# Performance work log

Hardware: AMD Instinct MI355X
Metric: run time of the kernel (lower is better)

The kernel has to match this reference:

```python
import jax, jax.numpy as jnp
import numpy as np

# 8 directional difference stencils (N, S, E, W, NE, SE, SW, NW), OIHW [8,1,3,3]
_WINDOWS = np.array([
    [[0, 1, 0], [0, -1, 0], [0, 0, 0]],
    [[0, 0, 0], [0, -1, 0], [0, 1, 0]],
    [[0, 0, 0], [0, -1, 1], [0, 0, 0]],
    [[0, 0, 0], [1, -1, 0], [0, 0, 0]],
    [[0, 0, 1], [0, -1, 0], [0, 0, 0]],
    [[0, 0, 0], [0, -1, 0], [0, 0, 1]],
    [[0, 0, 0], [0, -1, 0], [1, 0, 0]],
    [[1, 0, 0], [0, -1, 0], [0, 0, 0]],
], dtype=np.float32).reshape(8, 1, 3, 3)

ITERATIONS = 30  # int(self.iterations.item()) with init value 30.0


def setup_inputs() -> dict:
    key = jax.random.key(0)
    k1, k2, k3 = jax.random.split(key, 3)
    x = jax.random.normal(k1, (32, 3, 512, 512), dtype=jnp.float32)
    W_expand = jax.random.normal(k2, (3, 3, 1, 1), dtype=jnp.float32) * 0.3
    b_expand = jax.random.normal(k3, (3,), dtype=jnp.float32) * 0.1
    return {
        "x": x,
        "delta": jnp.float32(0.1),
        "kappa": jnp.float32(15.0),
        "W_expand": W_expand,
        "b_expand": b_expand,
    }


def reference(x, delta, kappa, W_expand, b_expand):
    K = jnp.asarray(_WINDOWS)  # [8,1,3,3]
    # axial directions weight 1, diagonal directions weight 1/(sqrt(2))^2 = 0.5
    dir_w = jnp.array([1.0, 1.0, 1.0, 1.0, 0.5, 0.5, 0.5, 0.5],
                      dtype=x.dtype).reshape(1, 8, 1, 1)

    # RGB -> luminance, [B,1,H,W]
    u = (0.299 * x[:, 0] + 0.587 * x[:, 1] + 0.114 * x[:, 2])[:, None]

    def step(u, _):
        # all 8 directional gradients in one grouped conv: [B,8,H,W]
        nabla = jax.lax.conv_general_dilated(
            u, K, window_strides=(1, 1), padding='SAME',
            dimension_numbers=('NCHW', 'OIHW', 'NCHW'))
        diff = 1.0 / (1.0 + (nabla / kappa) ** 2)  # Perona-Malik diffusivity
        upd = jnp.sum(dir_w * diff * nabla, axis=1, keepdims=True)
        return u + delta * upd, None

    u, _ = jax.lax.scan(step, u, None, length=ITERATIONS)

    # repeat to 3 channels then 1x1 conv (expand_channels)
    u_rgb = jnp.repeat(u, 3, axis=1)  # [B,3,H,W]
    out = jnp.einsum('oi,bihw->bohw', W_expand[:, :, 0, 0], u_rgb)
    out = out + b_expand[None, :, None, None]
    return out
```

## Files before the change

### kernel.cpp

```cpp
#include <hip/hip_runtime.h>

#define BATCH 32
#define HGT 512
#define WID 512
#define PLANE (HGT * WID)
#define NPIX (BATCH * PLANE)
#define BSTRIDE (3 * PLANE)
#define NQUAD (NPIX / 4)

#define RSLAB 32
#define SLABS (HGT / RSLAB)
#define FBLOCKS (BATCH * SLABS)
#define FT 512
#define NW 8

__device__ __forceinline__ float4 ld4(const float* p) {
    return *reinterpret_cast<const float4*>(p);
}
__device__ __forceinline__ void st4(float* p, float4 v) {
    *reinterpret_cast<float4*>(p) = v;
}

__device__ __forceinline__ float pm_flux(float d, float ik2) {
    return d * __builtin_amdgcn_rcpf(fmaf(d * d, ik2, 1.f));
}

struct RowState {
    float m[10];
    float pV[8], pSE[9], pSW[9];
};

__device__ __forceinline__ void load_row10(const float* __restrict__ buf, int row, int o,
                                           float m[10]) {
    const float* p = buf + row * WID + (o << 3);
    float4 lo = ld4(p);
    float4 hi = ld4(p + 4);
    float le = __shfl_up(hi.w, 1);
    float re = __shfl_down(lo.x, 1);
    m[0] = (o == 0) ? 0.f : le;
    m[1] = lo.x; m[2] = lo.y; m[3] = lo.z; m[4] = lo.w;
    m[5] = hi.x; m[6] = hi.y; m[7] = hi.z; m[8] = hi.w;
    m[9] = (o == 63) ? 0.f : re;
}

__device__ __forceinline__ void level10(const float a[10], const float b[10],
                                        float vF[8], float seF[9], float swF[9],
                                        float ik2) {
#pragma unroll
    for (int j = 0; j < 8; ++j) vF[j] = pm_flux(b[j + 1] - a[j + 1], ik2);
#pragma unroll
    for (int i = 0; i < 9; ++i) seF[i] = pm_flux(b[i + 1] - a[i], ik2);
#pragma unroll
    for (int i = 0; i < 9; ++i) swF[i] = pm_flux(b[i] - a[i + 1], ik2);
}

template <int MODE, int S>
__global__ __launch_bounds__(FT) __attribute__((amdgpu_waves_per_eu(4, 4)))
void pm_fusedk(const float* __restrict__ src, int sstr,
               float* __restrict__ dst, int dstr,
               const float* __restrict__ pdelta, const float* __restrict__ pkappa,
               const float* __restrict__ Wexp, const float* __restrict__ bexp) {
    constexpr int LR = RSLAB + 2 * S;
    __shared__ float buf[LR * WID];

    const int img  = blockIdx.x >> 4;
    const int slab = blockIdx.x & (SLABS - 1);
    const int H0   = slab * RSLAB;
    const int tid  = threadIdx.x;
    const int wave = tid >> 6;
    const int o    = tid & 63;

    const float delta = *pdelta;
    const float kappa = *pkappa;
    const float ik2 = __builtin_amdgcn_rcpf(kappa * kappa);

    const float* sb = src + (size_t)img * sstr;
    for (int i = tid; i < LR * (WID / 4); i += FT) {
        int row = i >> 7;
        int q   = i & 127;
        int g = H0 - S + row;
        float4 v = make_float4(0.f, 0.f, 0.f, 0.f);
        if ((unsigned)g < (unsigned)HGT) {
            const float* p = sb + g * WID + (q << 2);
            if (MODE == 0) {
                float4 r = ld4(p), gg = ld4(p + PLANE), bb = ld4(p + 2 * PLANE);
                v.x = fmaf(0.299f, r.x, fmaf(0.587f, gg.x, 0.114f * bb.x));
                v.y = fmaf(0.299f, r.y, fmaf(0.587f, gg.y, 0.114f * bb.y));
                v.z = fmaf(0.299f, r.z, fmaf(0.587f, gg.z, 0.114f * bb.z));
                v.w = fmaf(0.299f, r.w, fmaf(0.587f, gg.w, 0.114f * bb.w));
            } else {
                v = ld4(p);
            }
        }
        st4(buf + row * WID + (q << 2), v);
    }
    __syncthreads();

    float s0c = 0.f, s1c = 0.f, s2c = 0.f, b0c = 0.f, b1c = 0.f, b2c = 0.f;
    if (MODE == 2) {
        s0c = Wexp[0] + Wexp[1] + Wexp[2];
        s1c = Wexp[3] + Wexp[4] + Wexp[5];
        s2c = Wexp[6] + Wexp[7] + Wexp[8];
        b0c = bexp[0]; b1c = bexp[1]; b2c = bexp[2];
    }

    float* db = dst + (size_t)img * dstr;

    for (int s = 0; s < S; ++s) {
        const int tot = LR - 2 - 2 * s;
        const int bse = tot >> 3, rem = tot & 7;
        const int n   = bse + (wave < rem ? 1 : 0);
        const int st0 = s + 1 + wave * bse + (wave < rem ? wave : rem);
        const bool fin = (s == S - 1);

        RowState A, B;
        {
            float a10[10];
            load_row10(buf, st0 - 1, o, a10);
            load_row10(buf, st0, o, A.m);
            level10(a10, A.m, A.pV, A.pSE, A.pSW, ik2);
        }
        float4 f0 = make_float4(0, 0, 0, 0), f1 = f0, l0 = f0, l1 = f0;

        auto do_row = [&](RowState& CUR, RowState& NEXT, int i) {
            load_row10(buf, st0 + i + 1, o, NEXT.m);
            float hF[9];
#pragma unroll
            for (int t = 0; t < 9; ++t) hF[t] = pm_flux(CUR.m[t + 1] - CUR.m[t], ik2);
            level10(CUR.m, NEXT.m, NEXT.pV, NEXT.pSE, NEXT.pSW, ik2);
            float o8[8];
#pragma unroll
            for (int j = 0; j < 8; ++j) {
                float axial = NEXT.pV[j] - CUR.pV[j] + hF[j + 1] - hF[j];
                float diag  = NEXT.pSE[j + 1] + NEXT.pSW[j]
                            - CUR.pSE[j] - CUR.pSW[j + 1];
                o8[j] = fmaf(delta, fmaf(0.5f, diag, axial), CUR.m[j + 1]);
            }
            const int g = H0 - S + st0 + i;
            if ((unsigned)g >= (unsigned)HGT) {
#pragma unroll
                for (int j = 0; j < 8; ++j) o8[j] = 0.f;
            }
            float4 r0 = make_float4(o8[0], o8[1], o8[2], o8[3]);
            float4 r1 = make_float4(o8[4], o8[5], o8[6], o8[7]);
            if (fin) {
                float* p = db + (size_t)g * WID + (o << 3);
                if (MODE == 2) {
                    st4(p, make_float4(fmaf(s0c, r0.x, b0c), fmaf(s0c, r0.y, b0c),
                                       fmaf(s0c, r0.z, b0c), fmaf(s0c, r0.w, b0c)));
                    st4(p + 4, make_float4(fmaf(s0c, r1.x, b0c), fmaf(s0c, r1.y, b0c),
                                           fmaf(s0c, r1.z, b0c), fmaf(s0c, r1.w, b0c)));
                    st4(p + PLANE,
                        make_float4(fmaf(s1c, r0.x, b1c), fmaf(s1c, r0.y, b1c),
                                    fmaf(s1c, r0.z, b1c), fmaf(s1c, r0.w, b1c)));
                    st4(p + PLANE + 4,
                        make_float4(fmaf(s1c, r1.x, b1c), fmaf(s1c, r1.y, b1c),
                                    fmaf(s1c, r1.z, b1c), fmaf(s1c, r1.w, b1c)));
                    st4(p + 2 * PLANE,
                        make_float4(fmaf(s2c, r0.x, b2c), fmaf(s2c, r0.y, b2c),
                                    fmaf(s2c, r0.z, b2c), fmaf(s2c, r0.w, b2c)));
                    st4(p + 2 * PLANE + 4,
                        make_float4(fmaf(s2c, r1.x, b2c), fmaf(s2c, r1.y, b2c),
                                    fmaf(s2c, r1.z, b2c), fmaf(s2c, r1.w, b2c)));
                } else {
                    st4(p, r0);
                    st4(p + 4, r1);
                }
            } else if (i == 0) {
                f0 = r0; f1 = r1;
            } else if (i == n - 1) {
                l0 = r0; l1 = r1;
            } else {
                float* p = buf + (st0 + i) * WID + (o << 3);
                st4(p, r0);
                st4(p + 4, r1);
            }
        };

        for (int i = 0; i < n; i += 2) {
            do_row(A, B, i);
            if (i + 1 < n) do_row(B, A, i + 1);
        }

        if (!fin) {
            __syncthreads();
            float* p = buf + st0 * WID + (o << 3);
            st4(p, f0);
            st4(p + 4, f1);
            p = buf + (st0 + n - 1) * WID + (o << 3);
            st4(p, l0);
            st4(p + 4, l1);
            __syncthreads();
        }
    }
}

__global__ void expand_from(const float* __restrict__ usrc, int ustr,
                            float* __restrict__ out,
                            const float* __restrict__ Wexp,
                            const float* __restrict__ bexp) {
    int idx = blockIdx.x * blockDim.x + threadIdx.x;
    if (idx >= NQUAD) return;
    int b = idx / (PLANE / 4);
    int off = (idx - b * (PLANE / 4)) * 4;

    float4 u = ld4(usrc + (size_t)b * ustr + off);
    float s0 = Wexp[0] + Wexp[1] + Wexp[2];
    float s1 = Wexp[3] + Wexp[4] + Wexp[5];
    float s2 = Wexp[6] + Wexp[7] + Wexp[8];
    float b0 = bexp[0], b1 = bexp[1], b2 = bexp[2];

    size_t base = (size_t)b * BSTRIDE + off;
    st4(out + base, make_float4(fmaf(s0, u.x, b0), fmaf(s0, u.y, b0),
                                fmaf(s0, u.z, b0), fmaf(s0, u.w, b0)));
    st4(out + base + PLANE, make_float4(fmaf(s1, u.x, b1), fmaf(s1, u.y, b1),
                                        fmaf(s1, u.z, b1), fmaf(s1, u.w, b1)));
    st4(out + base + 2 * PLANE, make_float4(fmaf(s2, u.x, b2), fmaf(s2, u.y, b2),
                                            fmaf(s2, u.z, b2), fmaf(s2, u.w, b2)));
}

extern "C" void kernel_launch(void* const* d_in, const int* in_sizes, int n_in,
                              void* d_out, int out_size, void* d_ws, size_t ws_size,
                              hipStream_t stream) {
    const float* x      = (const float*)d_in[0];
    const float* pdelta = (const float*)d_in[1];
    const float* pkappa = (const float*)d_in[2];
    const float* Wexp   = (const float*)d_in[3];
    const float* bexp   = (const float*)d_in[4];
    float* out = (float*)d_out;

    const size_t need = (size_t)2 * NPIX * sizeof(float);
    if (ws_size >= need) {
        float* uA = (float*)d_ws;
        float* uB = uA + NPIX;
        pm_fusedk<0, 4><<<FBLOCKS, FT, 0, stream>>>(
            x, BSTRIDE, uA, PLANE, pdelta, pkappa, Wexp, bexp);
        float* s = uA;
        float* d = uB;
        for (int k = 0; k < 6; ++k) {
            pm_fusedk<1, 4><<<FBLOCKS, FT, 0, stream>>>(
                s, PLANE, d, PLANE, pdelta, pkappa, Wexp, bexp);
            float* t = s; s = d; d = t;
        }
        pm_fusedk<2, 2><<<FBLOCKS, FT, 0, stream>>>(
            s, PLANE, out, BSTRIDE, pdelta, pkappa, Wexp, bexp);
    } else {
        float* uA = out;
        float* uB = out + PLANE;
        pm_fusedk<0, 4><<<FBLOCKS, FT, 0, stream>>>(
            x, BSTRIDE, uA, BSTRIDE, pdelta, pkappa, Wexp, bexp);
        float* s = uA;
        float* d = uB;
        for (int k = 0; k < 6; ++k) {
            pm_fusedk<1, 4><<<FBLOCKS, FT, 0, stream>>>(
                s, BSTRIDE, d, BSTRIDE, pdelta, pkappa, Wexp, bexp);
            float* t = s; s = d; d = t;
        }
        pm_fusedk<1, 2><<<FBLOCKS, FT, 0, stream>>>(
            s, BSTRIDE, d, BSTRIDE, pdelta, pkappa, Wexp, bexp);
        const int block = 256;
        const int grid_q = (NQUAD + block - 1) / block;
        expand_from<<<grid_q, block, 0, stream>>>(d, BSTRIDE, out, Wexp, bexp);
    }
}
```

Baseline: 378.3 us.

## Swizzle row layout for conflict-free LDS loads and recompute fluxes per row

Stores each row in a swizzled layout: a thread's 8 pixels are split into two float4 halves 256 floats apart, so wave-wide LDS float4 accesses are contiguous and should avoid bank conflicts. The global intermediate buffer keeps this swizzled layout, and the final expand kernel un-swizzles it. The kernel also drops the carried vertical and diagonal flux state. It now recomputes all 8 directional fluxes per pixel and rotates three row registers, trading more rcp/ALU work for lower register pressure. Interior LDS write-back is delayed by one row so the row above is read before it is overwritten.

```diff
diff --git a/kernel.cpp b/kernel.cpp
--- a/kernel.cpp
+++ b/kernel.cpp
@@ -12,7 +12,6 @@
 #define SLABS (HGT / RSLAB)
 #define FBLOCKS (BATCH * SLABS)
 #define FT 512
-#define NW 8
 
 __device__ __forceinline__ float4 ld4(const float* p) {
     return *reinterpret_cast<const float4*>(p);
@@ -25,16 +24,15 @@
     return d * __builtin_amdgcn_rcpf(fmaf(d * d, ik2, 1.f));
 }
 
-struct RowState {
-    float m[10];
-    float pV[8], pSE[9], pSW[9];
-};
+__device__ __forceinline__ int swz(int q) {
+    return ((q & 1) << 8) + ((q >> 1) << 2);
+}
 
 __device__ __forceinline__ void load_row10(const float* __restrict__ buf, int row, int o,
                                            float m[10]) {
-    const float* p = buf + row * WID + (o << 3);
+    const float* p = buf + row * WID + (o << 2);
     float4 lo = ld4(p);
-    float4 hi = ld4(p + 4);
+    float4 hi = ld4(p + 256);
     float le = __shfl_up(hi.w, 1);
     float re = __shfl_down(lo.x, 1);
     m[0] = (o == 0) ? 0.f : le;
@@ -43,19 +41,8 @@
     m[9] = (o == 63) ? 0.f : re;
 }
 
-__device__ __forceinline__ void level10(const float a[10], const float b[10],
-                                        float vF[8], float seF[9], float swF[9],
-                                        float ik2) {
-#pragma unroll
-    for (int j = 0; j < 8; ++j) vF[j] = pm_flux(b[j + 1] - a[j + 1], ik2);
-#pragma unroll
-    for (int i = 0; i < 9; ++i) seF[i] = pm_flux(b[i + 1] - a[i], ik2);
-#pragma unroll
-    for (int i = 0; i < 9; ++i) swF[i] = pm_flux(b[i] - a[i + 1], ik2);
-}
-
 template <int MODE, int S>
-__global__ __launch_bounds__(FT) __attribute__((amdgpu_waves_per_eu(4, 4)))
+__global__ __launch_bounds__(FT, 4)
 void pm_fusedk(const float* __restrict__ src, int sstr,
                float* __restrict__ dst, int dstr,
                const float* __restrict__ pdelta, const float* __restrict__ pkappa,
@@ -92,7 +79,8 @@
                 v = ld4(p);
             }
         }
-        st4(buf + row * WID + (q << 2), v);
+        int dsto = (MODE == 0) ? swz(q) : (q << 2);
+        st4(buf + row * WID + dsto, v);
     }
     __syncthreads();
 
@@ -113,83 +101,93 @@
         const int st0 = s + 1 + wave * bse + (wave < rem ? wave : rem);
         const bool fin = (s == S - 1);
 
-        RowState A, B;
-        {
-            float a10[10];
-            load_row10(buf, st0 - 1, o, a10);
-            load_row10(buf, st0, o, A.m);
-            level10(a10, A.m, A.pV, A.pSE, A.pSW, ik2);
-        }
-        float4 f0 = make_float4(0, 0, 0, 0), f1 = f0, l0 = f0, l1 = f0;
-
-        auto do_row = [&](RowState& CUR, RowState& NEXT, int i) {
-            load_row10(buf, st0 + i + 1, o, NEXT.m);
+        float a[10], m[10], d[10];
+        load_row10(buf, st0 - 1, o, a);
+        load_row10(buf, st0, o, m);
+
+        float f8[8], l8[8], rp[8];
+
+        for (int i = 0; i < n; ++i) {
+            load_row10(buf, st0 + i + 1, o, d);
+
             float hF[9];
 #pragma unroll
-            for (int t = 0; t < 9; ++t) hF[t] = pm_flux(CUR.m[t + 1] - CUR.m[t], ik2);
-            level10(CUR.m, NEXT.m, NEXT.pV, NEXT.pSE, NEXT.pSW, ik2);
+            for (int t = 0; t < 9; ++t) hF[t] = pm_flux(m[t + 1] - m[t], ik2);
+
             float o8[8];
 #pragma unroll
             for (int j = 0; j < 8; ++j) {
-                float axial = NEXT.pV[j] - CUR.pV[j] + hF[j + 1] - hF[j];
-                float diag  = NEXT.pSE[j + 1] + NEXT.pSW[j]
-                            - CUR.pSE[j] - CUR.pSW[j + 1];
-                o8[j] = fmaf(delta, fmaf(0.5f, diag, axial), CUR.m[j + 1]);
-            }
+                float c = m[j + 1];
+                float ax = hF[j + 1] - hF[j];
+                ax += pm_flux(a[j + 1] - c, ik2);
+                ax += pm_flux(d[j + 1] - c, ik2);
+                float dg = pm_flux(a[j] - c, ik2);
+                dg += pm_flux(a[j + 2] - c, ik2);
+                dg += pm_flux(d[j] - c, ik2);
+                dg += pm_flux(d[j + 2] - c, ik2);
+                o8[j] = fmaf(delta, fmaf(0.5f, dg, ax), c);
+            }
+
             const int g = H0 - S + st0 + i;
             if ((unsigned)g >= (unsigned)HGT) {
 #pragma unroll
                 for (int j = 0; j < 8; ++j) o8[j] = 0.f;
             }
-            float4 r0 = make_float4(o8[0], o8[1], o8[2], o8[3]);
-            float4 r1 = make_float4(o8[4], o8[5], o8[6], o8[7]);
+
             if (fin) {
-                float* p = db + (size_t)g * WID + (o << 3);
                 if (MODE == 2) {
-                    st4(p, make_float4(fmaf(s0c, r0.x, b0c), fmaf(s0c, r0.y, b0c),
-                                       fmaf(s0c, r0.z, b0c), fmaf(s0c, r0.w, b0c)));
-                    st4(p + 4, make_float4(fmaf(s0c, r1.x, b0c), fmaf(s0c, r1.y, b0c),
-                                           fmaf(s0c, r1.z, b0c), fmaf(s0c, r1.w, b0c)));
+                    float* p = db + (size_t)g * WID + (o << 3);
+                    st4(p, make_float4(fmaf(s0c, o8[0], b0c), fmaf(s0c, o8[1], b0c),
+                                       fmaf(s0c, o8[2], b0c), fmaf(s0c, o8[3], b0c)));
+                    st4(p + 4, make_float4(fmaf(s0c, o8[4], b0c), fmaf(s0c, o8[5], b0c),
+                                           fmaf(s0c, o8[6], b0c), fmaf(s0c, o8[7], b0c)));
                     st4(p + PLANE,
-                        make_float4(fmaf(s1c, r0.x, b1c), fmaf(s1c, r0.y, b1c),
-                                    fmaf(s1c, r0.z, b1c), fmaf(s1c, r0.w, b1c)));
+                        make_float4(fmaf(s1c, o8[0], b1c), fmaf(s1c, o8[1], b1c),
+                                    fmaf(s1c, o8[2], b1c), fmaf(s1c, o8[3], b1c)));
                     st4(p + PLANE + 4,
-                        make_float4(fmaf(s1c, r1.x, b1c), fmaf(s1c, r1.y, b1c),
-                                    fmaf(s1c, r1.z, b1c), fmaf(s1c, r1.w, b1c)));
+                        make_float4(fmaf(s1c, o8[4], b1c), fmaf(s1c, o8[5], b1c),
+                                    fmaf(s1c, o8[6], b1c), fmaf(s1c, o8[7], b1c)));
                     st4(p + 2 * PLANE,
-                        make_float4(fmaf(s2c, r0.x, b2c), fmaf(s2c, r0.y, b2c),
-                                    fmaf(s2c, r0.z, b2c), fmaf(s2c, r0.w, b2c)));
+                        make_float4(fmaf(s2c, o8[0], b2c), fmaf(s2c, o8[1], b2c),
+                                    fmaf(s2c, o8[2], b2c), fmaf(s2c, o8[3], b2c)));
                     st4(p + 2 * PLANE + 4,
-                        make_float4(fmaf(s2c, r1.x, b2c), fmaf(s2c, r1.y, b2c),
-                                    fmaf(s2c, r1.z, b2c), fmaf(s2c, r1.w, b2c)));
+                        make_float4(fmaf(s2c, o8[4], b2c), fmaf(s2c, o8[5], b2c),
+                                    fmaf(s2c, o8[6], b2c), fmaf(s2c, o8[7], b2c)));
                 } else {
-                    st4(p, r0);
-                    st4(p + 4, r1);
+                    float* p = db + (size_t)g * WID + (o << 2);
+                    st4(p, make_float4(o8[0], o8[1], o8[2], o8[3]));
+                    st4(p + 256, make_float4(o8[4], o8[5], o8[6], o8[7]));
                 }
             } else if (i == 0) {
-                f0 = r0; f1 = r1;
-            } else if (i == n - 1) {
-                l0 = r0; l1 = r1;
+#pragma unroll
+                for (int j = 0; j < 8; ++j) f8[j] = o8[j];
             } else {
-                float* p = buf + (st0 + i) * WID + (o << 3);
-                st4(p, r0);
-                st4(p + 4, r1);
-            }
-        };
-
-        for (int i = 0; i < n; i += 2) {
-            do_row(A, B, i);
-            if (i + 1 < n) do_row(B, A, i + 1);
+                if (i >= 2) {
+                    float* p = buf + (st0 + i - 1) * WID + (o << 2);
+                    st4(p, make_float4(rp[0], rp[1], rp[2], rp[3]));
+                    st4(p + 256, make_float4(rp[4], rp[5], rp[6], rp[7]));
+                }
+                if (i == n - 1) {
+#pragma unroll
+                    for (int j = 0; j < 8; ++j) l8[j] = o8[j];
+                } else {
+#pragma unroll
+                    for (int j = 0; j < 8; ++j) rp[j] = o8[j];
+                }
+            }
+
+#pragma unroll
+            for (int t = 0; t < 10; ++t) { a[t] = m[t]; m[t] = d[t]; }
         }
 
         if (!fin) {
             __syncthreads();
-            float* p = buf + st0 * WID + (o << 3);
-            st4(p, f0);
-            st4(p + 4, f1);
-            p = buf + (st0 + n - 1) * WID + (o << 3);
-            st4(p, l0);
-            st4(p + 4, l1);
+            float* p = buf + st0 * WID + (o << 2);
+            st4(p, make_float4(f8[0], f8[1], f8[2], f8[3]));
+            st4(p + 256, make_float4(f8[4], f8[5], f8[6], f8[7]));
+            p = buf + (st0 + n - 1) * WID + (o << 2);
+            st4(p, make_float4(l8[0], l8[1], l8[2], l8[3]));
+            st4(p + 256, make_float4(l8[4], l8[5], l8[6], l8[7]));
             __syncthreads();
         }
     }
@@ -202,15 +200,17 @@
     int idx = blockIdx.x * blockDim.x + threadIdx.x;
     if (idx >= NQUAD) return;
     int b = idx / (PLANE / 4);
-    int off = (idx - b * (PLANE / 4)) * 4;
-
-    float4 u = ld4(usrc + (size_t)b * ustr + off);
+    int pq = idx - b * (PLANE / 4);
+    int row = pq >> 7;
+    int q   = pq & 127;
+
+    float4 u = ld4(usrc + (size_t)b * ustr + row * WID + swz(q));
     float s0 = Wexp[0] + Wexp[1] + Wexp[2];
     float s1 = Wexp[3] + Wexp[4] + Wexp[5];
     float s2 = Wexp[6] + Wexp[7] + Wexp[8];
     float b0 = bexp[0], b1 = bexp[1], b2 = bexp[2];
 
-    size_t base = (size_t)b * BSTRIDE + off;
+    size_t base = (size_t)b * BSTRIDE + row * WID + (q << 2);
     st4(out + base, make_float4(fmaf(s0, u.x, b0), fmaf(s0, u.y, b0),
                                 fmaf(s0, u.z, b0), fmaf(s0, u.w, b0)));
     st4(out + base + PLANE, make_float4(fmaf(s1, u.x, b1), fmaf(s1, u.y, b1),
```

Measured after the change: 442.4 us. 16.9% more time.
